# Kernel tuning notes

Hardware: AMD Instinct MI355X
Metric: run time of the kernel (lower is better)

Reference implementation:

```python
import jax, jax.numpy as jnp
import numpy as np

B, C, H, N, M = 4, 256, 4, 2048, 2048
D = C // H  # head_dim
BN_EPS = 1e-5


def conv1x1(W, b, x):
    # nn.Conv1d(Cin, Cout, kernel_size=1): x [B, Cin, N] -> [B, Cout, N]
    return jnp.einsum('oc,bcn->bon', W, x) + b[None, :, None]


def setup_inputs() -> dict:
    key = jax.random.key(0)
    ks = jax.random.split(key, 10)
    w = lambda k, shape: (jax.random.normal(k, shape, jnp.float32) * 0.05)
    return {
        'x1': jax.random.normal(ks[0], (B, C, N), jnp.float32),
        'x2': jax.random.normal(ks[1], (B, C, M), jnp.float32),
        'kv_mask': jax.random.randint(ks[2], (B, M), 0, 2).astype(bool),
        'Wq': w(ks[3], (C, C)), 'bq': jnp.zeros((C,), jnp.float32),
        'Wk': w(ks[4], (C, C)), 'bk': jnp.zeros((C,), jnp.float32),
        'Wv': w(ks[5], (C, C)), 'bv': jnp.zeros((C,), jnp.float32),
        'Wmh': w(ks[6], (C, C)), 'bmh': jnp.zeros((C,), jnp.float32),
        'W1': w(ks[7], (2 * C, 2 * C)), 'b1': jnp.zeros((2 * C,), jnp.float32),
        'bn_gamma': jnp.ones((2 * C,), jnp.float32),
        'bn_beta': jnp.zeros((2 * C,), jnp.float32),
        'bn_mean': jnp.zeros((2 * C,), jnp.float32),
        'bn_var': jnp.ones((2 * C,), jnp.float32),
        'W2': w(ks[8], (C, 2 * C)), 'b2': jnp.zeros((C,), jnp.float32),
    }


def reference(x1, x2, kv_mask, Wq, bq, Wk, bk, Wv, bv, Wmh, bmh,
              W1, b1, bn_gamma, bn_beta, bn_mean, bn_var, W2, b2):
    bsz = x1.shape[0]
    # 1x1-conv Q/K/V projections, reshaped to [B, H, D, N]
    q = conv1x1(Wq, bq, x1).reshape(bsz, H, D, -1)
    k = conv1x1(Wk, bk, x2).reshape(bsz, H, D, -1)
    v = conv1x1(Wv, bv, x2).reshape(bsz, H, D, -1)

    # full attention: scores [B, H, N, M]
    QK = jnp.einsum('bhdn,bhdm->bhnm', q, k)
    # masked_fill happens BEFORE the 1/sqrt(D) scaling in the original
    QK = jnp.where(kv_mask[:, None, None, :], QK, jnp.float32(-1e6))
    score = jax.nn.softmax(QK / np.float32(np.sqrt(D)), axis=-1)
    add_value = jnp.einsum('bhnm,bhdm->bhdn', score, v).reshape(bsz, H * D, -1)

    add_value = conv1x1(Wmh, bmh, add_value)

    # cat_filter: conv1x1 -> BatchNorm1d (inference stats) -> ReLU -> conv1x1
    cat = jnp.concatenate([x1, add_value], axis=1)  # [B, 2C, N]
    h = conv1x1(W1, b1, cat)
    h = (h - bn_mean[None, :, None]) / jnp.sqrt(bn_var[None, :, None] + BN_EPS)
    h = bn_gamma[None, :, None] * h + bn_beta[None, :, None]
    h = jax.nn.relu(h)
    return x1 + conv1x1(W2, b2, h)
```

## Files before the change

### kernel.cpp

```cpp
#include <hip/hip_runtime.h>
#include <hip/hip_bf16.h>

#define SEQN 2048
#define SEQM 2048
#define CDIM 256
#define NB   4
#define NH   4
#define RDYMAGIC 0x7A3F19C5u

using bf16x8 = __attribute__((ext_vector_type(8))) short;
using f32x4  = __attribute__((ext_vector_type(4))) float;

__device__ inline unsigned short f2bf(float x) {
    __hip_bfloat16 h = __float2bfloat16(x);
    return *reinterpret_cast<unsigned short*>(&h);
}

__global__ __launch_bounds__(256, 4) void qkv_k(
    const float* __restrict__ Wq, const float* __restrict__ Wk,
    const float* __restrict__ Wv,
    const float* __restrict__ x1, const float* __restrict__ x2,
    const float* __restrict__ bq, const float* __restrict__ bk,
    const float* __restrict__ bv,
    unsigned short* __restrict__ qbf, unsigned short* __restrict__ kbf,
    unsigned short* __restrict__ vbf,
    const int* __restrict__ kvm, int* __restrict__ pidx, int* __restrict__ mcnt,
    unsigned int* __restrict__ rdy, float qscale)
{
    __shared__ __align__(16) char qsm[35840];
    const int bid = blockIdx.x, tid = threadIdx.x;

    if (bid < NB) {
        int* sc = reinterpret_cast<int*>(qsm);
        const int b = bid;
        int loc[8], c = 0;
        #pragma unroll
        for (int e = 0; e < 8; ++e) {
            loc[e] = (kvm[(size_t)b * SEQM + tid * 8 + e] != 0) ? 1 : 0;
            c += loc[e];
        }
        sc[tid] = c;
        __syncthreads();
        for (int off = 1; off < 256; off <<= 1) {
            int v = (tid >= off) ? sc[tid - off] : 0;
            __syncthreads();
            sc[tid] += v;
            __syncthreads();
        }
        int p = sc[tid] - c;
        if (tid == 255) mcnt[b] = sc[255];
        #pragma unroll
        for (int e = 0; e < 8; ++e) {
            pidx[(size_t)b * SEQM + tid * 8 + e] = loc[e] ? p : -1;
            p += loc[e];
        }
        __threadfence();
        __syncthreads();
        if (tid == 0)
            __hip_atomic_store(&rdy[b], RDYMAGIC, __ATOMIC_RELEASE,
                               __HIP_MEMORY_SCOPE_AGENT);
        return;
    }

    const int g = bid - NB;
    const int z = g >> 8, t = g & 255;
    const int bx = t >> 7, by = t & 127;

    short (*At)[72] = reinterpret_cast<short(*)[72]>(qsm);
    float (*Ts)[68] = reinterpret_cast<float(*)[68]>(qsm + 18432);

    const float* W = (z == 0) ? Wq : (z == 1) ? Wk : Wv;
    const float* X = (z == 0) ? x1 : x2;
    const float* bias = (z == 0) ? bq : (z == 1) ? bk : bv;

    const int w = tid >> 6, l = tid & 63, lm = l & 15, lg = l >> 4;
    const int o0 = bx * 128, ng0 = by * 64;
    const int b = ng0 >> 11, n0 = ng0 & 2047;
    const int wo = (w >> 1) * 64, wn = (w & 1) * 32;

    f32x4 acc[4][2] = {};
    const int arow = tid >> 2, acol = (tid & 3) * 16;
    const int tr = tid >> 2, tc = (tid & 3) * 16;
    const int tg = (((tc >> 4) ^ ((tr >> 3) & 3)) << 4);

    for (int k0 = 0; k0 < 256; k0 += 64) {
        __syncthreads();
        #pragma unroll
        for (int p = 0; p < 2; ++p) {
            const float* s = &W[(size_t)(o0 + arow + 64 * p) * 256 + k0 + acol];
            unsigned int u[8];
            #pragma unroll
            for (int q = 0; q < 4; ++q) {
                float4 f = *reinterpret_cast<const float4*>(&s[4 * q]);
                u[2 * q]     = (unsigned int)f2bf(f.x) | ((unsigned int)f2bf(f.y) << 16);
                u[2 * q + 1] = (unsigned int)f2bf(f.z) | ((unsigned int)f2bf(f.w) << 16);
            }
            *reinterpret_cast<uint4*>(&At[arow + 64 * p][acol]) =
                make_uint4(u[0], u[1], u[2], u[3]);
            *reinterpret_cast<uint4*>(&At[arow + 64 * p][acol + 8]) =
                make_uint4(u[4], u[5], u[6], u[7]);
        }
        {
            const float* s = &X[((size_t)b * CDIM + k0 + tr) * SEQN + n0 + tc];
            #pragma unroll
            for (int q = 0; q < 4; ++q)
                *reinterpret_cast<float4*>(&Ts[tr][tg + 4 * q]) =
                    *reinterpret_cast<const float4*>(&s[4 * q]);
        }
        __syncthreads();
        #pragma unroll
        for (int kc = 0; kc < 2; ++kc) {
            bf16x8 a[4], bf[2];
            #pragma unroll
            for (int i = 0; i < 4; ++i)
                a[i] = *reinterpret_cast<const bf16x8*>(&At[wo + 16 * i + lm][kc * 32 + lg * 8]);
            #pragma unroll
            for (int j = 0; j < 2; ++j) {
                const int bk0 = kc * 32 + lg * 8;
                const int gcol = (((((wn >> 4) + j)) ^ ((bk0 >> 3) & 3)) << 4) | lm;
                union { unsigned int u[4]; bf16x8 v; } cv;
                #pragma unroll
                for (int e = 0; e < 4; ++e) {
                    float lo = Ts[bk0 + 2 * e][gcol];
                    float hi = Ts[bk0 + 2 * e + 1][gcol];
                    cv.u[e] = (unsigned int)f2bf(lo) | ((unsigned int)f2bf(hi) << 16);
                }
                bf[j] = cv.v;
            }
            #pragma unroll
            for (int i = 0; i < 4; ++i)
                #pragma unroll
                for (int j = 0; j < 2; ++j)
                    acc[i][j] = __builtin_amdgcn_mfma_f32_16x16x32_bf16(a[i], bf[j], acc[i][j], 0, 0, 0);
        }
    }

    if (z != 0) {
        if (tid == 0) {
            while (__hip_atomic_load(&rdy[b], __ATOMIC_ACQUIRE,
                                     __HIP_MEMORY_SCOPE_AGENT) != RDYMAGIC)
                __builtin_amdgcn_s_sleep(2);
        }
        __syncthreads();
    }

    #pragma unroll
    for (int j = 0; j < 2; ++j) {
        const int ng = ng0 + wn + 16 * j + lm;
        const int bb = ng >> 11, n = ng & 2047;
        const int pos = (z == 0) ? n : pidx[(size_t)bb * SEQM + n];
        #pragma unroll
        for (int i = 0; i < 4; ++i) {
            const int ob = o0 + wo + 16 * i + 4 * lg;
            float4 bv4 = *reinterpret_cast<const float4*>(&bias[ob]);
            float v[4] = {acc[i][j][0] + bv4.x, acc[i][j][1] + bv4.y,
                          acc[i][j][2] + bv4.z, acc[i][j][3] + bv4.w};
            if (z == 2) {
                if (pos >= 0) {
                    #pragma unroll
                    for (int r = 0; r < 4; ++r)
                        vbf[((size_t)bb * CDIM + ob + r) * SEQM + pos] = f2bf(v[r]);
                }
            } else if (pos >= 0) {
                const int hh = ob >> 6, dbase = ob & 63;
                const float sc_ = (z == 0) ? qscale : 1.0f;
                ushort4 pk;
                pk.x = f2bf(v[0] * sc_); pk.y = f2bf(v[1] * sc_);
                pk.z = f2bf(v[2] * sc_); pk.w = f2bf(v[3] * sc_);
                unsigned short* dst = (z == 0) ? qbf : kbf;
                *reinterpret_cast<ushort4*>(
                    &dst[(((size_t)bb * NH + hh) * SEQN + pos) * 64 + dbase]) = pk;
            }
        }
    }
}

__device__ void do_attn(char* smraw,
    const unsigned short* __restrict__ qbf, const unsigned short* __restrict__ kbf,
    const unsigned short* __restrict__ vbf, const int* __restrict__ mcntg,
    unsigned short* __restrict__ catT, int bx, int h, int b)
{
    short (*Ks)[64][64] = reinterpret_cast<short(*)[64][64]>(smraw);
    short (*Vs)[64][64] = reinterpret_cast<short(*)[64][64]>(smraw + 16384);
    unsigned int (*Ps)[16][36] = reinterpret_cast<unsigned int(*)[16][36]>(smraw + 32768);

    const int tid = threadIdx.x;
    const int w = tid >> 6, l = tid & 63;
    const int lm = l & 15, lg = l >> 4;
    const int n_base = bx * 64 + w * 16;
    const size_t bhN = (size_t)(b * NH + h) * SEQN;
    const size_t cBase = (size_t)b * CDIM + h * 64;

    const int mcnt = mcntg[b];
    const int ntiles = (mcnt + 63) >> 6;

    if (ntiles == 0) {
        #pragma unroll
        for (int r = 0; r < 4; ++r) {
            int n = n_base + 4 * lg + r;
            unsigned short* dst = &catT[((size_t)b * SEQN + n) * 512 + 256 + h * 64];
            #pragma unroll
            for (int t = 0; t < 4; ++t) dst[16 * t + lm] = 0;
        }
        return;
    }

    const size_t qrow = (bhN + n_base + lm) * 64;
    bf16x8 qa0 = *reinterpret_cast<const bf16x8*>(&qbf[qrow + lg * 8]);
    bf16x8 qa1 = *reinterpret_cast<const bf16x8*>(&qbf[qrow + 32 + lg * 8]);

    f32x4 oacc[4] = {};
    float mrun = -3.0e5f, lrun = 0.f;

    const int r0 = tid >> 3, c8 = (tid & 7) * 8;
    const int c8s = c8 ^ ((r0 & 7) << 3);
    const int colr0 = (lg * 8) ^ ((lm & 7) << 3);
    const int colr1 = (32 + lg * 8) ^ ((lm & 7) << 3);

    {
        bf16x8 kr[2], vr[2];
        #pragma unroll
        for (int p = 0; p < 2; ++p) {
            kr[p] = *reinterpret_cast<const bf16x8*>(&kbf[(bhN + r0 + 32 * p) * 64 + c8]);
            vr[p] = *reinterpret_cast<const bf16x8*>(&vbf[(cBase + r0 + 32 * p) * SEQM + c8]);
        }
        #pragma unroll
        for (int p = 0; p < 2; ++p) {
            *reinterpret_cast<bf16x8*>(&Ks[0][r0 + 32 * p][c8s]) = kr[p];
            *reinterpret_cast<bf16x8*>(&Vs[0][r0 + 32 * p][c8s]) = vr[p];
        }
    }
    __syncthreads();

    for (int t64 = 0; t64 < ntiles; ++t64) {
        const int cur = t64 & 1;
        const bool has_next = (t64 < ntiles - 1);
        const int m0n = (t64 + 1) * 64;

        bf16x8 kr[2], vr[2];
        if (has_next) {
            #pragma unroll
            for (int p = 0; p < 2; ++p) {
                kr[p] = *reinterpret_cast<const bf16x8*>(
                    &kbf[(bhN + m0n + r0 + 32 * p) * 64 + c8]);
                vr[p] = *reinterpret_cast<const bf16x8*>(
                    &vbf[(cBase + r0 + 32 * p) * SEQM + m0n + c8]);
            }
        }

        f32x4 sv[4];
        __builtin_amdgcn_s_setprio(1);
        #pragma unroll
        for (int t = 0; t < 4; ++t) {
            bf16x8 ka0 = *reinterpret_cast<const bf16x8*>(&Ks[cur][16 * t + lm][colr0]);
            bf16x8 ka1 = *reinterpret_cast<const bf16x8*>(&Ks[cur][16 * t + lm][colr1]);
            f32x4 z = {0.f, 0.f, 0.f, 0.f};
            z = __builtin_amdgcn_mfma_f32_16x16x32_bf16(ka0, qa0, z, 0, 0, 0);
            z = __builtin_amdgcn_mfma_f32_16x16x32_bf16(ka1, qa1, z, 0, 0, 0);
            sv[t] = z;
        }
        __builtin_amdgcn_s_setprio(0);

        float mx = fmaxf(fmaxf(fmaxf(sv[0][0], sv[0][1]), fmaxf(sv[0][2], sv[0][3])),
                         fmaxf(fmaxf(sv[1][0], sv[1][1]), fmaxf(sv[1][2], sv[1][3])));
        mx = fmaxf(mx, fmaxf(fmaxf(fmaxf(sv[2][0], sv[2][1]), fmaxf(sv[2][2], sv[2][3])),
                             fmaxf(fmaxf(sv[3][0], sv[3][1]), fmaxf(sv[3][2], sv[3][3]))));
        mx = fmaxf(mx, __shfl_xor(mx, 16));
        mx = fmaxf(mx, __shfl_xor(mx, 32));
        const bool grew = (mx > mrun);
        float mnew = fmaxf(mrun, mx);
        float scl = exp2f(mrun - mnew);
        mrun = mnew;

        float rsum = 0.f;
        const int mrem = mcnt - t64 * 64;
        if (mrem >= 64) {
            #pragma unroll
            for (int t = 0; t < 4; ++t) {
                float p0 = exp2f(sv[t][0] - mnew);
                float p1 = exp2f(sv[t][1] - mnew);
                float p2 = exp2f(sv[t][2] - mnew);
                float p3 = exp2f(sv[t][3] - mnew);
                rsum += (p0 + p1) + (p2 + p3);
                unsigned int u0 = __builtin_amdgcn_perm(
                    __float_as_uint(p1), __float_as_uint(p0), 0x07060302u);
                unsigned int u1 = __builtin_amdgcn_perm(
                    __float_as_uint(p3), __float_as_uint(p2), 0x07060302u);
                *reinterpret_cast<uint2*>(&Ps[w][lm][8 * t + 2 * lg]) = make_uint2(u0, u1);
            }
        } else {
            #pragma unroll
            for (int t = 0; t < 4; ++t) {
                const int mb = 16 * t + 4 * lg;
                float p0 = (mb + 0 < mrem) ? exp2f(sv[t][0] - mnew) : 0.f;
                float p1 = (mb + 1 < mrem) ? exp2f(sv[t][1] - mnew) : 0.f;
                float p2 = (mb + 2 < mrem) ? exp2f(sv[t][2] - mnew) : 0.f;
                float p3 = (mb + 3 < mrem) ? exp2f(sv[t][3] - mnew) : 0.f;
                rsum += (p0 + p1) + (p2 + p3);
                unsigned int u0 = __builtin_amdgcn_perm(
                    __float_as_uint(p1), __float_as_uint(p0), 0x07060302u);
                unsigned int u1 = __builtin_amdgcn_perm(
                    __float_as_uint(p3), __float_as_uint(p2), 0x07060302u);
                *reinterpret_cast<uint2*>(&Ps[w][lm][8 * t + 2 * lg]) = make_uint2(u0, u1);
            }
        }
        rsum += __shfl_xor(rsum, 16);
        rsum += __shfl_xor(rsum, 32);
        lrun = lrun * scl + rsum;

        if (__any(grew && scl < 1.f)) {
            float sr[4];
            #pragma unroll
            for (int r = 0; r < 4; ++r) sr[r] = __shfl(scl, 4 * lg + r);
            #pragma unroll
            for (int t = 0; t < 4; ++t)
                #pragma unroll
                for (int r = 0; r < 4; ++r)
                    oacc[t][r] *= sr[r];
        }

        bf16x8 pa0 = *reinterpret_cast<const bf16x8*>(&Ps[w][lm][4 * lg]);
        bf16x8 pa1 = *reinterpret_cast<const bf16x8*>(&Ps[w][lm][16 + 4 * lg]);
        __builtin_amdgcn_s_setprio(1);
        #pragma unroll
        for (int t = 0; t < 4; ++t) {
            bf16x8 vb0 = *reinterpret_cast<const bf16x8*>(&Vs[cur][16 * t + lm][colr0]);
            bf16x8 vb1 = *reinterpret_cast<const bf16x8*>(&Vs[cur][16 * t + lm][colr1]);
            oacc[t] = __builtin_amdgcn_mfma_f32_16x16x32_bf16(pa0, vb0, oacc[t], 0, 0, 0);
            oacc[t] = __builtin_amdgcn_mfma_f32_16x16x32_bf16(pa1, vb1, oacc[t], 0, 0, 0);
        }
        __builtin_amdgcn_s_setprio(0);

        if (has_next) {
            const int nxt = cur ^ 1;
            #pragma unroll
            for (int p = 0; p < 2; ++p) {
                *reinterpret_cast<bf16x8*>(&Ks[nxt][r0 + 32 * p][c8s]) = kr[p];
                *reinterpret_cast<bf16x8*>(&Vs[nxt][r0 + 32 * p][c8s]) = vr[p];
            }
        }
        __syncthreads();
    }

    #pragma unroll
    for (int r = 0; r < 4; ++r) {
        float rinv = 1.f / __shfl(lrun, 4 * lg + r);
        int n = n_base + 4 * lg + r;
        unsigned short* dst = &catT[((size_t)b * SEQN + n) * 512 + 256 + h * 64];
        #pragma unroll
        for (int t = 0; t < 4; ++t)
            dst[16 * t + lm] = f2bf(oacc[t][r] * rinv);
    }
}

__global__ __launch_bounds__(256) void fused2_k(
    const unsigned short* __restrict__ qbf, const unsigned short* __restrict__ kbf,
    const unsigned short* __restrict__ vbf, const int* __restrict__ mcnt,
    unsigned short* __restrict__ catT,
    const float* __restrict__ W1, const float* __restrict__ b1,
    const float* __restrict__ gamma, const float* __restrict__ beta,
    const float* __restrict__ mean, const float* __restrict__ var,
    const float* __restrict__ Wmh, const float* __restrict__ bmh,
    unsigned short* __restrict__ Acat, float* __restrict__ cvec,
    const float* __restrict__ x1,
    const float* __restrict__ W2, unsigned short* __restrict__ W2b)
{
    __shared__ __align__(16) char smraw[41984];
    const int bid = blockIdx.x, tid = threadIdx.x;

    if (bid < 512) {
        const int xcd = bid & 7, slot = bid >> 3;
        const int p2 = xcd * 2 + (slot >> 5);
        do_attn(smraw, qbf, kbf, vbf, mcnt, catT, slot & 31, p2 & 3, p2 >> 2);
    } else if (bid < 1024) {
        const int j = bid - 512;
        const int c = tid;
        const float s = gamma[j] * rsqrtf(var[j] + 1e-5f);
        const float* w1b = W1 + (size_t)j * 512 + 256;
        Acat[(size_t)j * 512 + c] = f2bf(s * W1[(size_t)j * 512 + c]);
        float acc = 0.f;
        for (int t = 0; t < 256; ++t)
            acc += w1b[t] * Wmh[(size_t)t * 256 + c];
        Acat[(size_t)j * 512 + 256 + c] = f2bf(s * acc);
        if (c == 0) {
            float ab = 0.f;
            for (int t = 0; t < 256; ++t) ab += w1b[t] * bmh[t];
            cvec[j] = s * (b1[j] + ab - mean[j]) + beta[j];
        }
    } else if (bid < 1536) {
        const int t = bid - 1024;
        float (*Ts)[68] = reinterpret_cast<float(*)[68]>(smraw);
        const int cx = t & 3, ny = (t >> 2) & 31, b = t >> 7;
        const int c0 = cx * 64, n0 = ny * 64;
        const int cr = tid >> 2, nc = (tid & 3) * 16;
        #pragma unroll
        for (int q = 0; q < 4; ++q) {
            float4 v = *reinterpret_cast<const float4*>(
                &x1[((size_t)b * CDIM + c0 + cr) * SEQN + n0 + nc + 4 * q]);
            *reinterpret_cast<float4*>(&Ts[cr][nc + 4 * q]) = v;
        }
        __syncthreads();
        const int nr = tid >> 2, cc = (tid & 3) * 16;
        unsigned short tmp[16];
        #pragma unroll
        for (int e = 0; e < 16; ++e) tmp[e] = f2bf(Ts[cc + e][nr]);
        unsigned short* dp = &catT[((size_t)(b * SEQN + n0 + nr)) * 512 + c0 + cc];
        #pragma unroll
        for (int q = 0; q < 4; ++q)
            *reinterpret_cast<ushort4*>(&dp[4 * q]) = *reinterpret_cast<ushort4*>(&tmp[4 * q]);
    } else {
        const int cid = bid - 1536;
        const int idx = (cid * 256 + tid) * 4;
        float4 v = *reinterpret_cast<const float4*>(&W2[idx]);
        ushort4 p; p.x = f2bf(v.x); p.y = f2bf(v.y); p.z = f2bf(v.z); p.w = f2bf(v.w);
        *reinterpret_cast<ushort4*>(&W2b[idx]) = p;
    }
}

__global__ __launch_bounds__(256) void gemm2_k(
    const unsigned short* __restrict__ W, const unsigned short* __restrict__ X,
    const float* __restrict__ bias, unsigned short* __restrict__ obf)
{
    __shared__ short At[128][72];
    __shared__ short Bt[64][72];
    const int tid = threadIdx.x;
    const int w = tid >> 6, l = tid & 63, lm = l & 15, lg = l >> 4;
    const int g = blockIdx.x;
    const int bx = g >> 7, by = g & 127;
    const int o0 = bx * 128, ng0 = by * 64;
    const int wo = (w >> 1) * 64, wn = (w & 1) * 32;

    f32x4 acc[4][2] = {};
    const int arow = tid >> 2, acol = (tid & 3) * 16;

    for (int k0 = 0; k0 < 512; k0 += 64) {
        __syncthreads();
        #pragma unroll
        for (int p = 0; p < 2; ++p) {
            const unsigned short* s = &W[(size_t)(o0 + arow + 64 * p) * 512 + k0 + acol];
            *reinterpret_cast<bf16x8*>(&At[arow + 64 * p][acol]) =
                *reinterpret_cast<const bf16x8*>(s);
            *reinterpret_cast<bf16x8*>(&At[arow + 64 * p][acol + 8]) =
                *reinterpret_cast<const bf16x8*>(s + 8);
        }
        {
            const unsigned short* s = &X[(size_t)(ng0 + arow) * 512 + k0 + acol];
            *reinterpret_cast<bf16x8*>(&Bt[arow][acol]) =
                *reinterpret_cast<const bf16x8*>(s);
            *reinterpret_cast<bf16x8*>(&Bt[arow][acol + 8]) =
                *reinterpret_cast<const bf16x8*>(s + 8);
        }
        __syncthreads();
        #pragma unroll
        for (int kc = 0; kc < 2; ++kc) {
            bf16x8 a[4], bf[2];
            #pragma unroll
            for (int i = 0; i < 4; ++i)
                a[i] = *reinterpret_cast<const bf16x8*>(&At[wo + 16 * i + lm][kc * 32 + lg * 8]);
            #pragma unroll
            for (int j = 0; j < 2; ++j)
                bf[j] = *reinterpret_cast<const bf16x8*>(&Bt[wn + 16 * j + lm][kc * 32 + lg * 8]);
            #pragma unroll
            for (int i = 0; i < 4; ++i)
                #pragma unroll
                for (int j = 0; j < 2; ++j)
                    acc[i][j] = __builtin_amdgcn_mfma_f32_16x16x32_bf16(a[i], bf[j], acc[i][j], 0, 0, 0);
        }
    }

    #pragma unroll
    for (int j = 0; j < 2; ++j) {
        const int ng = ng0 + wn + 16 * j + lm;
        #pragma unroll
        for (int i = 0; i < 4; ++i) {
            const int ob = o0 + wo + 16 * i + 4 * lg;
            float4 bv = *reinterpret_cast<const float4*>(&bias[ob]);
            ushort4 pk;
            pk.x = f2bf(fmaxf(acc[i][j][0] + bv.x, 0.f));
            pk.y = f2bf(fmaxf(acc[i][j][1] + bv.y, 0.f));
            pk.z = f2bf(fmaxf(acc[i][j][2] + bv.z, 0.f));
            pk.w = f2bf(fmaxf(acc[i][j][3] + bv.w, 0.f));
            *reinterpret_cast<ushort4*>(&obf[(size_t)ng * 512 + ob]) = pk;
        }
    }
}

__global__ __launch_bounds__(256) void gemm3_k(
    const unsigned short* __restrict__ W, const unsigned short* __restrict__ X,
    const float* __restrict__ bias, const float* __restrict__ res,
    float* __restrict__ ofp)
{
    __shared__ short At[64][72];
    __shared__ short Bt[64][72];
    const int tid = threadIdx.x;
    const int w = tid >> 6, l = tid & 63, lm = l & 15, lg = l >> 4;
    const int g = blockIdx.x;
    const int bx = g >> 7, by = g & 127;
    const int o0 = bx * 64, ng0 = by * 64;
    const int wo = (w >> 1) * 32, wn = (w & 1) * 32;

    f32x4 acc[2][2] = {};
    const int arow = tid >> 2, acol = (tid & 3) * 16;

    for (int k0 = 0; k0 < 512; k0 += 64) {
        __syncthreads();
        {
            const unsigned short* s = &W[(size_t)(o0 + arow) * 512 + k0 + acol];
            *reinterpret_cast<bf16x8*>(&At[arow][acol]) =
                *reinterpret_cast<const bf16x8*>(s);
            *reinterpret_cast<bf16x8*>(&At[arow][acol + 8]) =
                *reinterpret_cast<const bf16x8*>(s + 8);
        }
        {
            const unsigned short* s = &X[(size_t)(ng0 + arow) * 512 + k0 + acol];
            *reinterpret_cast<bf16x8*>(&Bt[arow][acol]) =
                *reinterpret_cast<const bf16x8*>(s);
            *reinterpret_cast<bf16x8*>(&Bt[arow][acol + 8]) =
                *reinterpret_cast<const bf16x8*>(s + 8);
        }
        __syncthreads();
        #pragma unroll
        for (int kc = 0; kc < 2; ++kc) {
            bf16x8 a[2], bf[2];
            #pragma unroll
            for (int i = 0; i < 2; ++i)
                a[i] = *reinterpret_cast<const bf16x8*>(&At[wo + 16 * i + lm][kc * 32 + lg * 8]);
            #pragma unroll
            for (int j = 0; j < 2; ++j)
                bf[j] = *reinterpret_cast<const bf16x8*>(&Bt[wn + 16 * j + lm][kc * 32 + lg * 8]);
            #pragma unroll
            for (int i = 0; i < 2; ++i)
                #pragma unroll
                for (int j = 0; j < 2; ++j)
                    acc[i][j] = __builtin_amdgcn_mfma_f32_16x16x32_bf16(a[i], bf[j], acc[i][j], 0, 0, 0);
        }
    }

    #pragma unroll
    for (int j = 0; j < 2; ++j) {
        const int ng = ng0 + wn + 16 * j + lm;
        const int b = ng >> 11, n = ng & 2047;
        #pragma unroll
        for (int i = 0; i < 2; ++i) {
            const int ob = o0 + wo + 16 * i + 4 * lg;
            float4 bv = *reinterpret_cast<const float4*>(&bias[ob]);
            float v[4] = {acc[i][j][0] + bv.x, acc[i][j][1] + bv.y,
                          acc[i][j][2] + bv.z, acc[i][j][3] + bv.w};
            #pragma unroll
            for (int r = 0; r < 4; ++r) {
                size_t ad = ((size_t)b * CDIM + ob + r) * SEQN + n;
                ofp[ad] = v[r] + res[ad];
            }
        }
    }
}

extern "C" void kernel_launch(void* const* d_in, const int* in_sizes, int n_in,
                              void* d_out, int out_size, void* d_ws, size_t ws_size,
                              hipStream_t stream)
{
    (void)in_sizes; (void)n_in; (void)out_size; (void)ws_size;
    const float* x1    = (const float*)d_in[0];
    const float* x2    = (const float*)d_in[1];
    const int*   kvm   = (const int*)  d_in[2];
    const float* Wq    = (const float*)d_in[3];
    const float* bq    = (const float*)d_in[4];
    const float* Wk    = (const float*)d_in[5];
    const float* bk    = (const float*)d_in[6];
    const float* Wv    = (const float*)d_in[7];
    const float* bv    = (const float*)d_in[8];
    const float* Wmh   = (const float*)d_in[9];
    const float* bmh   = (const float*)d_in[10];
    const float* W1    = (const float*)d_in[11];
    const float* b1    = (const float*)d_in[12];
    const float* gamma = (const float*)d_in[13];
    const float* beta  = (const float*)d_in[14];
    const float* mean  = (const float*)d_in[15];
    const float* var   = (const float*)d_in[16];
    const float* W2    = (const float*)d_in[17];
    const float* b2    = (const float*)d_in[18];
    float* out = (float*)d_out;

    const size_t act = (size_t)NB * CDIM * SEQN;
    unsigned short* ws    = (unsigned short*)d_ws;
    unsigned short* qbf   = ws;
    unsigned short* kbf   = qbf   + act;
    unsigned short* vbf   = kbf   + act;
    unsigned short* catT  = vbf   + act;
    unsigned short* hbuf  = catT  + 2 * act;
    unsigned short* W2b   = hbuf  + 2 * act;
    unsigned short* Acat  = W2b   + 131072;
    float*          cvec  = (float*)(Acat + 262144);
    int*            pidx  = (int*)(cvec + 512);
    int*            mcnt  = pidx + (size_t)NB * SEQM;
    unsigned int*   rdy   = (unsigned int*)(mcnt + 16);

    const float qscale = 0.125f * 1.44269504088896f;

    qkv_k<<<dim3(NB + 768), dim3(256), 0, stream>>>(
        Wq, Wk, Wv, x1, x2, bq, bk, bv, qbf, kbf, vbf,
        kvm, pidx, mcnt, rdy, qscale);

    fused2_k<<<dim3(1664), dim3(256), 0, stream>>>(
        qbf, kbf, vbf, mcnt, catT,
        W1, b1, gamma, beta, mean, var, Wmh, bmh, Acat, cvec,
        x1, W2, W2b);

    gemm2_k<<<dim3(512), dim3(256), 0, stream>>>(Acat, catT, cvec, hbuf);

    gemm3_k<<<dim3(512), dim3(256), 0, stream>>>(W2b, hbuf, b2, x1, out);
}
```

Measured before the change: 74.30 us.

## Fuse the two FFN GEMM kernels with per-tile atomic counters for the dependency

Merges the cat-filter first GEMM (with bias/BN/ReLU) and the second GEMM (with residual) into one kernel. Each block computes its 128-channel slice of h, bumps a per-column-tile counter, then spins until all four channel slices for that column tile are done before running the second GEMM. The counters are reset in the first kernel. This removes one kernel launch and the gap between the two kernels. In exchange it adds spin-waiting, which could stall or deadlock if the dependent blocks are not co-resident, and it relies on the spin cap as a fallback.

```diff
diff --git a/kernel.cpp b/kernel.cpp
--- a/kernel.cpp
+++ b/kernel.cpp
@@ -25,12 +25,14 @@
     unsigned short* __restrict__ qbf, unsigned short* __restrict__ kbf,
     unsigned short* __restrict__ vbf,
     const int* __restrict__ kvm, int* __restrict__ pidx, int* __restrict__ mcnt,
-    unsigned int* __restrict__ rdy, float qscale)
+    unsigned int* __restrict__ rdy, unsigned int* __restrict__ hcnt,
+    float qscale)
 {
     __shared__ __align__(16) char qsm[35840];
     const int bid = blockIdx.x, tid = threadIdx.x;
 
     if (bid < NB) {
+        if (bid == 0 && tid < 128) hcnt[tid] = 0;
         int* sc = reinterpret_cast<int*>(qsm);
         const int b = bid;
         int loc[8], c = 0;
@@ -417,139 +419,143 @@
     }
 }
 
-__global__ __launch_bounds__(256) void gemm2_k(
-    const unsigned short* __restrict__ W, const unsigned short* __restrict__ X,
-    const float* __restrict__ bias, unsigned short* __restrict__ obf)
+__global__ __launch_bounds__(256) void gemm23_k(
+    const unsigned short* __restrict__ Acat, const float* __restrict__ cvec,
+    const unsigned short* __restrict__ W2b, const float* __restrict__ b2,
+    const float* __restrict__ x1, const unsigned short* __restrict__ catT,
+    unsigned short* __restrict__ hbuf, float* __restrict__ out,
+    unsigned int* __restrict__ hcnt)
 {
     __shared__ short At[128][72];
     __shared__ short Bt[64][72];
     const int tid = threadIdx.x;
     const int w = tid >> 6, l = tid & 63, lm = l & 15, lg = l >> 4;
-    const int g = blockIdx.x;
-    const int bx = g >> 7, by = g & 127;
-    const int o0 = bx * 128, ng0 = by * 64;
-    const int wo = (w >> 1) * 64, wn = (w & 1) * 32;
-
-    f32x4 acc[4][2] = {};
     const int arow = tid >> 2, acol = (tid & 3) * 16;
-
-    for (int k0 = 0; k0 < 512; k0 += 64) {
-        __syncthreads();
-        #pragma unroll
-        for (int p = 0; p < 2; ++p) {
-            const unsigned short* s = &W[(size_t)(o0 + arow + 64 * p) * 512 + k0 + acol];
-            *reinterpret_cast<bf16x8*>(&At[arow + 64 * p][acol]) =
-                *reinterpret_cast<const bf16x8*>(s);
-            *reinterpret_cast<bf16x8*>(&At[arow + 64 * p][acol + 8]) =
-                *reinterpret_cast<const bf16x8*>(s + 8);
-        }
-        {
-            const unsigned short* s = &X[(size_t)(ng0 + arow) * 512 + k0 + acol];
-            *reinterpret_cast<bf16x8*>(&Bt[arow][acol]) =
-                *reinterpret_cast<const bf16x8*>(s);
-            *reinterpret_cast<bf16x8*>(&Bt[arow][acol + 8]) =
-                *reinterpret_cast<const bf16x8*>(s + 8);
-        }
-        __syncthreads();
-        #pragma unroll
-        for (int kc = 0; kc < 2; ++kc) {
-            bf16x8 a[4], bf[2];
-            #pragma unroll
-            for (int i = 0; i < 4; ++i)
-                a[i] = *reinterpret_cast<const bf16x8*>(&At[wo + 16 * i + lm][kc * 32 + lg * 8]);
-            #pragma unroll
-            for (int j = 0; j < 2; ++j)
-                bf[j] = *reinterpret_cast<const bf16x8*>(&Bt[wn + 16 * j + lm][kc * 32 + lg * 8]);
-            #pragma unroll
-            for (int i = 0; i < 4; ++i)
+    const int bid = blockIdx.x;
+    const int bx = bid >> 7, by = bid & 127;
+    const int ng0 = by * 64;
+
+    {
+        const int o0 = bx * 128;
+        const int wo = (w >> 1) * 64, wn = (w & 1) * 32;
+        f32x4 acc[4][2] = {};
+        for (int k0 = 0; k0 < 512; k0 += 64) {
+            __syncthreads();
+            #pragma unroll
+            for (int p = 0; p < 2; ++p) {
+                const unsigned short* s = &Acat[(size_t)(o0 + arow + 64 * p) * 512 + k0 + acol];
+                *reinterpret_cast<bf16x8*>(&At[arow + 64 * p][acol]) =
+                    *reinterpret_cast<const bf16x8*>(s);
+                *reinterpret_cast<bf16x8*>(&At[arow + 64 * p][acol + 8]) =
+                    *reinterpret_cast<const bf16x8*>(s + 8);
+            }
+            {
+                const unsigned short* s = &catT[(size_t)(ng0 + arow) * 512 + k0 + acol];
+                *reinterpret_cast<bf16x8*>(&Bt[arow][acol]) =
+                    *reinterpret_cast<const bf16x8*>(s);
+                *reinterpret_cast<bf16x8*>(&Bt[arow][acol + 8]) =
+                    *reinterpret_cast<const bf16x8*>(s + 8);
+            }
+            __syncthreads();
+            #pragma unroll
+            for (int kc = 0; kc < 2; ++kc) {
+                bf16x8 a[4], bf[2];
+                #pragma unroll
+                for (int i = 0; i < 4; ++i)
+                    a[i] = *reinterpret_cast<const bf16x8*>(&At[wo + 16 * i + lm][kc * 32 + lg * 8]);
                 #pragma unroll
                 for (int j = 0; j < 2; ++j)
-                    acc[i][j] = __builtin_amdgcn_mfma_f32_16x16x32_bf16(a[i], bf[j], acc[i][j], 0, 0, 0);
-        }
-    }
-
-    #pragma unroll
-    for (int j = 0; j < 2; ++j) {
-        const int ng = ng0 + wn + 16 * j + lm;
-        #pragma unroll
-        for (int i = 0; i < 4; ++i) {
-            const int ob = o0 + wo + 16 * i + 4 * lg;
-            float4 bv = *reinterpret_cast<const float4*>(&bias[ob]);
-            ushort4 pk;
-            pk.x = f2bf(fmaxf(acc[i][j][0] + bv.x, 0.f));
-            pk.y = f2bf(fmaxf(acc[i][j][1] + bv.y, 0.f));
-            pk.z = f2bf(fmaxf(acc[i][j][2] + bv.z, 0.f));
-            pk.w = f2bf(fmaxf(acc[i][j][3] + bv.w, 0.f));
-            *reinterpret_cast<ushort4*>(&obf[(size_t)ng * 512 + ob]) = pk;
-        }
-    }
-}
-
-__global__ __launch_bounds__(256) void gemm3_k(
-    const unsigned short* __restrict__ W, const unsigned short* __restrict__ X,
-    const float* __restrict__ bias, const float* __restrict__ res,
-    float* __restrict__ ofp)
-{
-    __shared__ short At[64][72];
-    __shared__ short Bt[64][72];
-    const int tid = threadIdx.x;
-    const int w = tid >> 6, l = tid & 63, lm = l & 15, lg = l >> 4;
-    const int g = blockIdx.x;
-    const int bx = g >> 7, by = g & 127;
-    const int o0 = bx * 64, ng0 = by * 64;
-    const int wo = (w >> 1) * 32, wn = (w & 1) * 32;
-
-    f32x4 acc[2][2] = {};
-    const int arow = tid >> 2, acol = (tid & 3) * 16;
-
-    for (int k0 = 0; k0 < 512; k0 += 64) {
-        __syncthreads();
-        {
-            const unsigned short* s = &W[(size_t)(o0 + arow) * 512 + k0 + acol];
-            *reinterpret_cast<bf16x8*>(&At[arow][acol]) =
-                *reinterpret_cast<const bf16x8*>(s);
-            *reinterpret_cast<bf16x8*>(&At[arow][acol + 8]) =
-                *reinterpret_cast<const bf16x8*>(s + 8);
-        }
-        {
-            const unsigned short* s = &X[(size_t)(ng0 + arow) * 512 + k0 + acol];
-            *reinterpret_cast<bf16x8*>(&Bt[arow][acol]) =
-                *reinterpret_cast<const bf16x8*>(s);
-            *reinterpret_cast<bf16x8*>(&Bt[arow][acol + 8]) =
-                *reinterpret_cast<const bf16x8*>(s + 8);
-        }
-        __syncthreads();
-        #pragma unroll
-        for (int kc = 0; kc < 2; ++kc) {
-            bf16x8 a[2], bf[2];
-            #pragma unroll
-            for (int i = 0; i < 2; ++i)
-                a[i] = *reinterpret_cast<const bf16x8*>(&At[wo + 16 * i + lm][kc * 32 + lg * 8]);
-            #pragma unroll
-            for (int j = 0; j < 2; ++j)
-                bf[j] = *reinterpret_cast<const bf16x8*>(&Bt[wn + 16 * j + lm][kc * 32 + lg * 8]);
-            #pragma unroll
-            for (int i = 0; i < 2; ++i)
+                    bf[j] = *reinterpret_cast<const bf16x8*>(&Bt[wn + 16 * j + lm][kc * 32 + lg * 8]);
+                #pragma unroll
+                for (int i = 0; i < 4; ++i)
+                    #pragma unroll
+                    for (int j = 0; j < 2; ++j)
+                        acc[i][j] = __builtin_amdgcn_mfma_f32_16x16x32_bf16(a[i], bf[j], acc[i][j], 0, 0, 0);
+            }
+        }
+        #pragma unroll
+        for (int j = 0; j < 2; ++j) {
+            const int ng = ng0 + wn + 16 * j + lm;
+            #pragma unroll
+            for (int i = 0; i < 4; ++i) {
+                const int ob = o0 + wo + 16 * i + 4 * lg;
+                float4 bv = *reinterpret_cast<const float4*>(&cvec[ob]);
+                ushort4 pk;
+                pk.x = f2bf(fmaxf(acc[i][j][0] + bv.x, 0.f));
+                pk.y = f2bf(fmaxf(acc[i][j][1] + bv.y, 0.f));
+                pk.z = f2bf(fmaxf(acc[i][j][2] + bv.z, 0.f));
+                pk.w = f2bf(fmaxf(acc[i][j][3] + bv.w, 0.f));
+                *reinterpret_cast<ushort4*>(&hbuf[(size_t)ng * 512 + ob]) = pk;
+            }
+        }
+        __syncthreads();
+        if (tid == 0) {
+            __threadfence();
+            atomicAdd(&hcnt[by], 1u);
+        }
+    }
+
+    if (tid == 0) {
+        int sp = 0;
+        while (__hip_atomic_load(&hcnt[by], __ATOMIC_ACQUIRE,
+                                 __HIP_MEMORY_SCOPE_AGENT) < 4u && sp < 4000000) {
+            __builtin_amdgcn_s_sleep(8);
+            ++sp;
+        }
+    }
+
+    {
+        const int o0 = bx * 64;
+        const int wo = (w >> 1) * 32, wn = (w & 1) * 32;
+        f32x4 acc[2][2] = {};
+        for (int k0 = 0; k0 < 512; k0 += 64) {
+            __syncthreads();
+            {
+                const unsigned short* s = &W2b[(size_t)(o0 + arow) * 512 + k0 + acol];
+                *reinterpret_cast<bf16x8*>(&At[arow][acol]) =
+                    *reinterpret_cast<const bf16x8*>(s);
+                *reinterpret_cast<bf16x8*>(&At[arow][acol + 8]) =
+                    *reinterpret_cast<const bf16x8*>(s + 8);
+            }
+            {
+                const unsigned short* s = &hbuf[(size_t)(ng0 + arow) * 512 + k0 + acol];
+                *reinterpret_cast<bf16x8*>(&Bt[arow][acol]) =
+                    *reinterpret_cast<const bf16x8*>(s);
+                *reinterpret_cast<bf16x8*>(&Bt[arow][acol + 8]) =
+                    *reinterpret_cast<const bf16x8*>(s + 8);
+            }
+            __syncthreads();
+            #pragma unroll
+            for (int kc = 0; kc < 2; ++kc) {
+                bf16x8 a[2], bf[2];
+                #pragma unroll
+                for (int i = 0; i < 2; ++i)
+                    a[i] = *reinterpret_cast<const bf16x8*>(&At[wo + 16 * i + lm][kc * 32 + lg * 8]);
                 #pragma unroll
                 for (int j = 0; j < 2; ++j)
-                    acc[i][j] = __builtin_amdgcn_mfma_f32_16x16x32_bf16(a[i], bf[j], acc[i][j], 0, 0, 0);
-        }
-    }
-
-    #pragma unroll
-    for (int j = 0; j < 2; ++j) {
-        const int ng = ng0 + wn + 16 * j + lm;
-        const int b = ng >> 11, n = ng & 2047;
-        #pragma unroll
-        for (int i = 0; i < 2; ++i) {
-            const int ob = o0 + wo + 16 * i + 4 * lg;
-            float4 bv = *reinterpret_cast<const float4*>(&bias[ob]);
-            float v[4] = {acc[i][j][0] + bv.x, acc[i][j][1] + bv.y,
-                          acc[i][j][2] + bv.z, acc[i][j][3] + bv.w};
-            #pragma unroll
-            for (int r = 0; r < 4; ++r) {
-                size_t ad = ((size_t)b * CDIM + ob + r) * SEQN + n;
-                ofp[ad] = v[r] + res[ad];
+                    bf[j] = *reinterpret_cast<const bf16x8*>(&Bt[wn + 16 * j + lm][kc * 32 + lg * 8]);
+                #pragma unroll
+                for (int i = 0; i < 2; ++i)
+                    #pragma unroll
+                    for (int j = 0; j < 2; ++j)
+                        acc[i][j] = __builtin_amdgcn_mfma_f32_16x16x32_bf16(a[i], bf[j], acc[i][j], 0, 0, 0);
+            }
+        }
+        #pragma unroll
+        for (int j = 0; j < 2; ++j) {
+            const int ng = ng0 + wn + 16 * j + lm;
+            const int b = ng >> 11, n = ng & 2047;
+            #pragma unroll
+            for (int i = 0; i < 2; ++i) {
+                const int ob = o0 + wo + 16 * i + 4 * lg;
+                float4 bv = *reinterpret_cast<const float4*>(&b2[ob]);
+                float v[4] = {acc[i][j][0] + bv.x, acc[i][j][1] + bv.y,
+                              acc[i][j][2] + bv.z, acc[i][j][3] + bv.w};
+                #pragma unroll
+                for (int r = 0; r < 4; ++r) {
+                    size_t ad = ((size_t)b * CDIM + ob + r) * SEQN + n;
+                    out[ad] = v[r] + x1[ad];
+                }
             }
         }
     }
@@ -594,19 +600,19 @@
     int*            pidx  = (int*)(cvec + 512);
     int*            mcnt  = pidx + (size_t)NB * SEQM;
     unsigned int*   rdy   = (unsigned int*)(mcnt + 16);
+    unsigned int*   hcnt  = rdy + 16;
 
     const float qscale = 0.125f * 1.44269504088896f;
 
     qkv_k<<<dim3(NB + 768), dim3(256), 0, stream>>>(
         Wq, Wk, Wv, x1, x2, bq, bk, bv, qbf, kbf, vbf,
-        kvm, pidx, mcnt, rdy, qscale);
+        kvm, pidx, mcnt, rdy, hcnt, qscale);
 
     fused2_k<<<dim3(1664), dim3(256), 0, stream>>>(
         qbf, kbf, vbf, mcnt, catT,
         W1, b1, gamma, beta, mean, var, Wmh, bmh, Acat, cvec,
         x1, W2, W2b);
 
-    gemm2_k<<<dim3(512), dim3(256), 0, stream>>>(Acat, catT, cvec, hbuf);
-
-    gemm3_k<<<dim3(512), dim3(256), 0, stream>>>(W2b, hbuf, b2, x1, out);
+    gemm23_k<<<dim3(512), dim3(256), 0, stream>>>(
+        Acat, cvec, W2b, b2, x1, catT, hbuf, out, hcnt);
 }
```

Result: slower. 99.20 us (+33.5%).

## Process 128-key tiles per iteration with single-buffered K/V in attention

Applied to the files above, without the earlier changes.

The flash-attention loop now handles 128 keys per iteration instead of 64, so it runs half as many softmax max/rescale steps and loop iterations. K/V shared-memory tiles are single-buffered at the larger width, with two barriers around the register-staged refill. The P staging buffer is widened, which grows LDS from about 41KB to about 49KB. This may lower occupancy and adds a second barrier per iteration. Padded masked keys also round up to 128 instead of 64, so more wasted compute is possible.

```diff
diff --git a/kernel.cpp b/kernel.cpp
--- a/kernel.cpp
+++ b/kernel.cpp
@@ -180,9 +180,10 @@
     const unsigned short* __restrict__ vbf, const int* __restrict__ mcntg,
     unsigned short* __restrict__ catT, int bx, int h, int b)
 {
-    short (*Ks)[64][64] = reinterpret_cast<short(*)[64][64]>(smraw);
-    short (*Vs)[64][64] = reinterpret_cast<short(*)[64][64]>(smraw + 16384);
-    unsigned int (*Ps)[16][36] = reinterpret_cast<unsigned int(*)[16][36]>(smraw + 32768);
+    short (*Ks)[64]  = reinterpret_cast<short(*)[64]>(smraw);
+    short (*Vs)[128] = reinterpret_cast<short(*)[128]>(smraw + 16384);
+    unsigned int (*Ps)[16][68] =
+        reinterpret_cast<unsigned int(*)[16][68]>(smraw + 32768);
 
     const int tid = threadIdx.x;
     const int w = tid >> 6, l = tid & 63;
@@ -192,9 +193,9 @@
     const size_t cBase = (size_t)b * CDIM + h * 64;
 
     const int mcnt = mcntg[b];
-    const int ntiles = (mcnt + 63) >> 6;
-
-    if (ntiles == 0) {
+    const int npairs = (mcnt + 127) >> 7;
+
+    if (npairs == 0) {
         #pragma unroll
         for (int r = 0; r < 4; ++r) {
             int n = n_base + 4 * lg + r;
@@ -213,47 +214,53 @@
     float mrun = -3.0e5f, lrun = 0.f;
 
     const int r0 = tid >> 3, c8 = (tid & 7) * 8;
-    const int c8s = c8 ^ ((r0 & 7) << 3);
+    const int swz = (r0 & 7) << 3;
     const int colr0 = (lg * 8) ^ ((lm & 7) << 3);
     const int colr1 = (32 + lg * 8) ^ ((lm & 7) << 3);
 
     {
-        bf16x8 kr[2], vr[2];
-        #pragma unroll
-        for (int p = 0; p < 2; ++p) {
-            kr[p] = *reinterpret_cast<const bf16x8*>(&kbf[(bhN + r0 + 32 * p) * 64 + c8]);
-            vr[p] = *reinterpret_cast<const bf16x8*>(&vbf[(cBase + r0 + 32 * p) * SEQM + c8]);
-        }
-        #pragma unroll
-        for (int p = 0; p < 2; ++p) {
-            *reinterpret_cast<bf16x8*>(&Ks[0][r0 + 32 * p][c8s]) = kr[p];
-            *reinterpret_cast<bf16x8*>(&Vs[0][r0 + 32 * p][c8s]) = vr[p];
-        }
+        #pragma unroll
+        for (int p = 0; p < 4; ++p) {
+            bf16x8 kv = *reinterpret_cast<const bf16x8*>(
+                &kbf[(bhN + r0 + 32 * p) * 64 + c8]);
+            *reinterpret_cast<bf16x8*>(&Ks[r0 + 32 * p][c8 ^ swz]) = kv;
+        }
+        #pragma unroll
+        for (int p = 0; p < 2; ++p)
+            #pragma unroll
+            for (int hh = 0; hh < 2; ++hh) {
+                bf16x8 vv = *reinterpret_cast<const bf16x8*>(
+                    &vbf[(cBase + r0 + 32 * p) * SEQM + 64 * hh + c8]);
+                *reinterpret_cast<bf16x8*>(
+                    &Vs[r0 + 32 * p][64 * hh + (c8 ^ swz)]) = vv;
+            }
     }
     __syncthreads();
 
-    for (int t64 = 0; t64 < ntiles; ++t64) {
-        const int cur = t64 & 1;
-        const bool has_next = (t64 < ntiles - 1);
-        const int m0n = (t64 + 1) * 64;
-
-        bf16x8 kr[2], vr[2];
+    for (int pr = 0; pr < npairs; ++pr) {
+        const bool has_next = (pr < npairs - 1);
+        const int nb = (pr + 1) * 128;
+
+        bf16x8 kr[4], vr[4];
         if (has_next) {
             #pragma unroll
-            for (int p = 0; p < 2; ++p) {
+            for (int p = 0; p < 4; ++p)
                 kr[p] = *reinterpret_cast<const bf16x8*>(
-                    &kbf[(bhN + m0n + r0 + 32 * p) * 64 + c8]);
-                vr[p] = *reinterpret_cast<const bf16x8*>(
-                    &vbf[(cBase + r0 + 32 * p) * SEQM + m0n + c8]);
-            }
-        }
-
-        f32x4 sv[4];
+                    &kbf[(bhN + nb + r0 + 32 * p) * 64 + c8]);
+            #pragma unroll
+            for (int p = 0; p < 2; ++p)
+                #pragma unroll
+                for (int hh = 0; hh < 2; ++hh)
+                    vr[2 * p + hh] = *reinterpret_cast<const bf16x8*>(
+                        &vbf[(cBase + r0 + 32 * p) * SEQM + nb + 64 * hh + c8]);
+        }
+
+        f32x4 sv[8];
         __builtin_amdgcn_s_setprio(1);
         #pragma unroll
-        for (int t = 0; t < 4; ++t) {
-            bf16x8 ka0 = *reinterpret_cast<const bf16x8*>(&Ks[cur][16 * t + lm][colr0]);
-            bf16x8 ka1 = *reinterpret_cast<const bf16x8*>(&Ks[cur][16 * t + lm][colr1]);
+        for (int t = 0; t < 8; ++t) {
+            bf16x8 ka0 = *reinterpret_cast<const bf16x8*>(&Ks[16 * t + lm][colr0]);
+            bf16x8 ka1 = *reinterpret_cast<const bf16x8*>(&Ks[16 * t + lm][colr1]);
             f32x4 z = {0.f, 0.f, 0.f, 0.f};
             z = __builtin_amdgcn_mfma_f32_16x16x32_bf16(ka0, qa0, z, 0, 0, 0);
             z = __builtin_amdgcn_mfma_f32_16x16x32_bf16(ka1, qa1, z, 0, 0, 0);
@@ -261,10 +268,12 @@
         }
         __builtin_amdgcn_s_setprio(0);
 
-        float mx = fmaxf(fmaxf(fmaxf(sv[0][0], sv[0][1]), fmaxf(sv[0][2], sv[0][3])),
-                         fmaxf(fmaxf(sv[1][0], sv[1][1]), fmaxf(sv[1][2], sv[1][3])));
-        mx = fmaxf(mx, fmaxf(fmaxf(fmaxf(sv[2][0], sv[2][1]), fmaxf(sv[2][2], sv[2][3])),
-                             fmaxf(fmaxf(sv[3][0], sv[3][1]), fmaxf(sv[3][2], sv[3][3]))));
+        float mt[8];
+        #pragma unroll
+        for (int t = 0; t < 8; ++t)
+            mt[t] = fmaxf(fmaxf(fmaxf(sv[t][0], sv[t][1]), sv[t][2]), sv[t][3]);
+        float mx = fmaxf(fmaxf(fmaxf(mt[0], mt[1]), fmaxf(mt[2], mt[3])),
+                         fmaxf(fmaxf(mt[4], mt[5]), fmaxf(mt[6], mt[7])));
         mx = fmaxf(mx, __shfl_xor(mx, 16));
         mx = fmaxf(mx, __shfl_xor(mx, 32));
         const bool grew = (mx > mrun);
@@ -273,10 +282,10 @@
         mrun = mnew;
 
         float rsum = 0.f;
-        const int mrem = mcnt - t64 * 64;
-        if (mrem >= 64) {
-            #pragma unroll
-            for (int t = 0; t < 4; ++t) {
+        const int mrem = mcnt - pr * 128;
+        if (mrem >= 128) {
+            #pragma unroll
+            for (int t = 0; t < 8; ++t) {
                 float p0 = exp2f(sv[t][0] - mnew);
                 float p1 = exp2f(sv[t][1] - mnew);
                 float p2 = exp2f(sv[t][2] - mnew);
@@ -290,7 +299,7 @@
             }
         } else {
             #pragma unroll
-            for (int t = 0; t < 4; ++t) {
+            for (int t = 0; t < 8; ++t) {
                 const int mb = 16 * t + 4 * lg;
                 float p0 = (mb + 0 < mrem) ? exp2f(sv[t][0] - mnew) : 0.f;
                 float p1 = (mb + 1 < mrem) ? exp2f(sv[t][1] - mnew) : 0.f;
@@ -319,27 +328,36 @@
                     oacc[t][r] *= sr[r];
         }
 
-        bf16x8 pa0 = *reinterpret_cast<const bf16x8*>(&Ps[w][lm][4 * lg]);
-        bf16x8 pa1 = *reinterpret_cast<const bf16x8*>(&Ps[w][lm][16 + 4 * lg]);
+        bf16x8 pa[4];
+        #pragma unroll
+        for (int s = 0; s < 4; ++s)
+            pa[s] = *reinterpret_cast<const bf16x8*>(&Ps[w][lm][16 * s + 4 * lg]);
         __builtin_amdgcn_s_setprio(1);
         #pragma unroll
         for (int t = 0; t < 4; ++t) {
-            bf16x8 vb0 = *reinterpret_cast<const bf16x8*>(&Vs[cur][16 * t + lm][colr0]);
-            bf16x8 vb1 = *reinterpret_cast<const bf16x8*>(&Vs[cur][16 * t + lm][colr1]);
-            oacc[t] = __builtin_amdgcn_mfma_f32_16x16x32_bf16(pa0, vb0, oacc[t], 0, 0, 0);
-            oacc[t] = __builtin_amdgcn_mfma_f32_16x16x32_bf16(pa1, vb1, oacc[t], 0, 0, 0);
+            #pragma unroll
+            for (int s = 0; s < 4; ++s) {
+                const int off = (s & 1) * 32 + lg * 8;
+                const int col = 64 * (s >> 1) + (off ^ ((lm & 7) << 3));
+                bf16x8 vb = *reinterpret_cast<const bf16x8*>(&Vs[16 * t + lm][col]);
+                oacc[t] = __builtin_amdgcn_mfma_f32_16x16x32_bf16(pa[s], vb, oacc[t], 0, 0, 0);
+            }
         }
         __builtin_amdgcn_s_setprio(0);
 
         if (has_next) {
-            const int nxt = cur ^ 1;
-            #pragma unroll
-            for (int p = 0; p < 2; ++p) {
-                *reinterpret_cast<bf16x8*>(&Ks[nxt][r0 + 32 * p][c8s]) = kr[p];
-                *reinterpret_cast<bf16x8*>(&Vs[nxt][r0 + 32 * p][c8s]) = vr[p];
-            }
-        }
-        __syncthreads();
+            __syncthreads();
+            #pragma unroll
+            for (int p = 0; p < 4; ++p)
+                *reinterpret_cast<bf16x8*>(&Ks[r0 + 32 * p][c8 ^ swz]) = kr[p];
+            #pragma unroll
+            for (int p = 0; p < 2; ++p)
+                #pragma unroll
+                for (int hh = 0; hh < 2; ++hh)
+                    *reinterpret_cast<bf16x8*>(
+                        &Vs[r0 + 32 * p][64 * hh + (c8 ^ swz)]) = vr[2 * p + hh];
+            __syncthreads();
+        }
     }
 
     #pragma unroll
@@ -365,7 +383,7 @@
     const float* __restrict__ x1,
     const float* __restrict__ W2, unsigned short* __restrict__ W2b)
 {
-    __shared__ __align__(16) char smraw[41984];
+    __shared__ __align__(16) char smraw[50176];
     const int bid = blockIdx.x, tid = threadIdx.x;
 
     if (bid < 512) {
```

After: 83.18 us. +12.0%, slower.

## Read K/V fragments directly from global memory, drop LDS double buffering

Applied to the files above, without the earlier changes.

Removes the shared-memory double-buffered staging of K and V tiles in the attention path. Each wave now loads its MFMA operands straight from global memory (relying on L1/L2), which eliminates the per-tile __syncthreads and cuts LDS use from about 41 KB to 17 KB, allowing more resident blocks. The cost is that the four waves each fetch the same K/V data redundantly, with no explicit prefetch overlapping loads and compute, so global and cache traffic and load latency rise.

```diff
diff --git a/kernel.cpp b/kernel.cpp
--- a/kernel.cpp
+++ b/kernel.cpp
@@ -180,9 +180,7 @@
     const unsigned short* __restrict__ vbf, const int* __restrict__ mcntg,
     unsigned short* __restrict__ catT, int bx, int h, int b)
 {
-    short (*Ks)[64][64] = reinterpret_cast<short(*)[64][64]>(smraw);
-    short (*Vs)[64][64] = reinterpret_cast<short(*)[64][64]>(smraw + 16384);
-    unsigned int (*Ps)[16][36] = reinterpret_cast<unsigned int(*)[16][36]>(smraw + 32768);
+    unsigned int (*Ps)[16][36] = reinterpret_cast<unsigned int(*)[16][36]>(smraw);
 
     const int tid = threadIdx.x;
     const int w = tid >> 6, l = tid & 63;
@@ -212,48 +210,16 @@
     f32x4 oacc[4] = {};
     float mrun = -3.0e5f, lrun = 0.f;
 
-    const int r0 = tid >> 3, c8 = (tid & 7) * 8;
-    const int c8s = c8 ^ ((r0 & 7) << 3);
-    const int colr0 = (lg * 8) ^ ((lm & 7) << 3);
-    const int colr1 = (32 + lg * 8) ^ ((lm & 7) << 3);
-
-    {
-        bf16x8 kr[2], vr[2];
-        #pragma unroll
-        for (int p = 0; p < 2; ++p) {
-            kr[p] = *reinterpret_cast<const bf16x8*>(&kbf[(bhN + r0 + 32 * p) * 64 + c8]);
-            vr[p] = *reinterpret_cast<const bf16x8*>(&vbf[(cBase + r0 + 32 * p) * SEQM + c8]);
-        }
-        #pragma unroll
-        for (int p = 0; p < 2; ++p) {
-            *reinterpret_cast<bf16x8*>(&Ks[0][r0 + 32 * p][c8s]) = kr[p];
-            *reinterpret_cast<bf16x8*>(&Vs[0][r0 + 32 * p][c8s]) = vr[p];
-        }
-    }
-    __syncthreads();
-
     for (int t64 = 0; t64 < ntiles; ++t64) {
-        const int cur = t64 & 1;
-        const bool has_next = (t64 < ntiles - 1);
-        const int m0n = (t64 + 1) * 64;
-
-        bf16x8 kr[2], vr[2];
-        if (has_next) {
-            #pragma unroll
-            for (int p = 0; p < 2; ++p) {
-                kr[p] = *reinterpret_cast<const bf16x8*>(
-                    &kbf[(bhN + m0n + r0 + 32 * p) * 64 + c8]);
-                vr[p] = *reinterpret_cast<const bf16x8*>(
-                    &vbf[(cBase + r0 + 32 * p) * SEQM + m0n + c8]);
-            }
-        }
+        const int m0 = t64 * 64;
 
         f32x4 sv[4];
         __builtin_amdgcn_s_setprio(1);
         #pragma unroll
         for (int t = 0; t < 4; ++t) {
-            bf16x8 ka0 = *reinterpret_cast<const bf16x8*>(&Ks[cur][16 * t + lm][colr0]);
-            bf16x8 ka1 = *reinterpret_cast<const bf16x8*>(&Ks[cur][16 * t + lm][colr1]);
+            const unsigned short* kp = &kbf[(bhN + m0 + 16 * t + lm) * 64 + lg * 8];
+            bf16x8 ka0 = *reinterpret_cast<const bf16x8*>(kp);
+            bf16x8 ka1 = *reinterpret_cast<const bf16x8*>(kp + 32);
             f32x4 z = {0.f, 0.f, 0.f, 0.f};
             z = __builtin_amdgcn_mfma_f32_16x16x32_bf16(ka0, qa0, z, 0, 0, 0);
             z = __builtin_amdgcn_mfma_f32_16x16x32_bf16(ka1, qa1, z, 0, 0, 0);
@@ -273,7 +239,7 @@
         mrun = mnew;
 
         float rsum = 0.f;
-        const int mrem = mcnt - t64 * 64;
+        const int mrem = mcnt - m0;
         if (mrem >= 64) {
             #pragma unroll
             for (int t = 0; t < 4; ++t) {
@@ -324,22 +290,13 @@
         __builtin_amdgcn_s_setprio(1);
         #pragma unroll
         for (int t = 0; t < 4; ++t) {
-            bf16x8 vb0 = *reinterpret_cast<const bf16x8*>(&Vs[cur][16 * t + lm][colr0]);
-            bf16x8 vb1 = *reinterpret_cast<const bf16x8*>(&Vs[cur][16 * t + lm][colr1]);
+            const unsigned short* vp = &vbf[(cBase + 16 * t + lm) * SEQM + m0 + lg * 8];
+            bf16x8 vb0 = *reinterpret_cast<const bf16x8*>(vp);
+            bf16x8 vb1 = *reinterpret_cast<const bf16x8*>(vp + 32);
             oacc[t] = __builtin_amdgcn_mfma_f32_16x16x32_bf16(pa0, vb0, oacc[t], 0, 0, 0);
             oacc[t] = __builtin_amdgcn_mfma_f32_16x16x32_bf16(pa1, vb1, oacc[t], 0, 0, 0);
         }
         __builtin_amdgcn_s_setprio(0);
-
-        if (has_next) {
-            const int nxt = cur ^ 1;
-            #pragma unroll
-            for (int p = 0; p < 2; ++p) {
-                *reinterpret_cast<bf16x8*>(&Ks[nxt][r0 + 32 * p][c8s]) = kr[p];
-                *reinterpret_cast<bf16x8*>(&Vs[nxt][r0 + 32 * p][c8s]) = vr[p];
-            }
-        }
-        __syncthreads();
     }
 
     #pragma unroll
@@ -365,7 +322,7 @@
     const float* __restrict__ x1,
     const float* __restrict__ W2, unsigned short* __restrict__ W2b)
 {
-    __shared__ __align__(16) char smraw[41984];
+    __shared__ __align__(16) char smraw[17408];
     const int bid = blockIdx.x, tid = threadIdx.x;
 
     if (bid < 512) {
```

New measurement: 110.8 us. 49.2% more time.
